# Kernel tuning notes

Measured on AMD Instinct MI355X. Metric: run time of the kernel, lower is better.

The kernel has to match this reference:

```python
import jax, jax.numpy as jnp
import numpy as np

D = 1024
POOL_SIZES = [1024, 512, 256, 128, 64]  # n_pos=32*32 -> n_codes=64
CODEBOOK_SIZE = 512
BATCH = 32
W_SCALE = 0.03125  # ~1/sqrt(D) so pre-softmax logits stay O(1)


def setup_inputs() -> dict:
    key = jax.random.key(0)
    ks = jax.random.split(key, 7)
    x = jax.random.normal(ks[0], (BATCH, POOL_SIZES[0], D), dtype=jnp.float32)
    queries = jax.random.normal(ks[1], (len(POOL_SIZES), POOL_SIZES[0], D), dtype=jnp.float32)
    wq = jax.random.normal(ks[2], (len(POOL_SIZES), D, D), dtype=jnp.float32) * W_SCALE
    wk = jax.random.normal(ks[3], (len(POOL_SIZES), D, D), dtype=jnp.float32) * W_SCALE
    wv = jax.random.normal(ks[4], (len(POOL_SIZES), D, D), dtype=jnp.float32) * W_SCALE
    wo = jax.random.normal(ks[5], (len(POOL_SIZES), D, D), dtype=jnp.float32) * W_SCALE
    codebook = jax.random.normal(ks[6], (CODEBOOK_SIZE, D), dtype=jnp.float32)
    return {"x": x, "queries": queries, "wq": wq, "wk": wk, "wv": wv, "wo": wo, "codebook": codebook}


def reference(x, queries, wq, wk, wv, wo, codebook):
    # StackedPooling: S -> 1024 -> 512 -> 256 -> 128 -> 64 via AttentionPool stages
    scale = D ** (-0.5)
    h = x
    for i, K in enumerate(POOL_SIZES):
        q = queries[i, :K, :] @ wq[i]              # [K, D] learned queries, q_proj
        k = jnp.einsum("bsd,de->bse", h, wk[i])    # [B, S, D]
        v = jnp.einsum("bsd,de->bse", h, wv[i])    # [B, S, D]
        logits = jnp.einsum("kd,bsd->bks", q, k) * scale
        attn = jax.nn.softmax(logits, axis=-1)     # [B, K, S]
        pooled = jnp.einsum("bks,bsd->bkd", attn, v)
        h = jnp.einsum("bkd,de->bke", pooled, wo[i])  # [B, K, D]
    # VQ codebook quantization: nearest code per latent (squared L2)
    z = h                                          # [B, n_codes, D]
    d2 = (jnp.sum(z * z, axis=-1, keepdims=True)
          - 2.0 * jnp.einsum("bkd,cd->bkc", z, codebook)
          + jnp.sum(codebook * codebook, axis=-1))  # [B, n_codes, C]
    idx = jnp.argmin(d2, axis=-1)                  # [B, n_codes] int
    z_q = codebook[idx]                            # [B, n_codes, D]
    # straight-through estimator
    out = z + jax.lax.stop_gradient(z_q - z)
    return out
```

## Files before the change

### kernel.cpp

```cpp
#include <hip/hip_runtime.h>


#define MB (1024ull * 1024ull)

typedef unsigned short u16;
typedef __attribute__((ext_vector_type(4))) float f32x4;
typedef __bf16 bf16x8 __attribute__((ext_vector_type(8)));

__device__ __forceinline__ u16 f2bf(float f) {
  unsigned u = __float_as_uint(f);
  unsigned r = u + 0x7FFFu + ((u >> 16) & 1u);
  return (u16)(r >> 16);
}
__device__ __forceinline__ float bf2f(u16 h) {
  return __uint_as_float(((unsigned)h) << 16);
}

typedef __attribute__((address_space(1))) const void GASV;
typedef __attribute__((address_space(3))) void LASV;
__device__ __forceinline__ void async16(const void* g, void* l) {
  __builtin_amdgcn_global_load_lds((GASV*)g, (LASV*)l, 16, 0, 0);
}

__device__ __forceinline__ int xcd_swz(int bid, int nwg) {
  const int q8 = nwg >> 3, r8 = nwg & 7;
  const int xcd = bid & 7, idx = bid >> 3;
  return (xcd < r8 ? xcd * (q8 + 1) : r8 * (q8 + 1) + (xcd - r8) * q8) + idx;
}

template<int MODE>
__global__ __launch_bounds__(512, 1)
void gemm_c(const u16* __restrict__ A, const u16* __restrict__ B,
            float* __restrict__ Cf, u16* __restrict__ Cb,
            int M, int N, int KLEN, int ld,
            long long sA, long long sB, long long sC, int ldc, float alpha,
            int nxt, int nyt)
{
  __shared__ u16 lds[65536];
  const int tid  = threadIdx.x;
  const int lane = tid & 63;
  const int w    = tid >> 6;
  const int wr   = w >> 2, wc = w & 3;

  const int wg = xcd_swz((int)blockIdx.x, (int)gridDim.x);
  const int bx = wg % nxt;
  const int by = (wg / nxt) % nyt;
  const int bz = wg / (nxt * nyt);

  const int m0 = by * 256, n0 = bx * 256;
  const u16* Ab = A + (size_t)bz * sA;
  const u16* Bb = B + (size_t)bz * sB;
  const int NT = KLEN >> 6;

  f32x4 acc[8][4] = {};

  const int Rl  = tid >> 2;
  const int sgs = (tid & 3) ^ ((tid >> 3) & 3);
  int ra0 = m0 + Rl;        ra0 = ra0 < M - 1 ? ra0 : M - 1;
  int ra1 = m0 + 128 + Rl;  ra1 = ra1 < M - 1 ? ra1 : M - 1;
  int rb0 = n0 + Rl;        rb0 = rb0 < N - 1 ? rb0 : N - 1;
  int rb1 = n0 + 128 + Rl;  rb1 = rb1 < N - 1 ? rb1 : N - 1;
  const u16* gA0 = Ab + (size_t)ra0 * ld + (sgs << 3);
  const u16* gA1 = Ab + (size_t)ra1 * ld + (sgs << 3);
  const u16* gB0 = Bb + (size_t)rb0 * ld + (sgs << 3);
  const u16* gB1 = Bb + (size_t)rb1 * ld + (sgs << 3);
  const int ldst = (w << 4) * 32;

  auto stageH = [&](int mat, int buf, int kh, int tile) {
    const int tt = tile < NT ? tile : NT - 1;
    const int kc = (tt << 6) + (kh << 5);
    u16* d = &lds[(mat << 15) + (buf << 14) + (kh << 13) + ldst];
    if (mat == 0) { async16(gA0 + kc, d); async16(gA1 + kc, d + 4096); }
    else          { async16(gB0 + kc, d); async16(gB1 + kc, d + 4096); }
  };

  const int rsel = lane & 15;
  const int ksub = lane >> 4;
  const int sw   = ksub ^ ((rsel >> 1) & 3);
  const u16* ldsA = &lds[(wr * 128 + rsel) * 32 + sw * 8];
  const u16* ldsB = &lds[32768 + (wc * 64 + rsel) * 32 + sw * 8];

  auto phase = [&](int buf, int kh, int mh, bf16x8* b,
                   int smat, int sbuf, int skh, int stile, int vm) {
    bf16x8 a[4];
    if (mh == 0) {
#pragma unroll
      for (int ni = 0; ni < 4; ++ni)
        b[ni] = *(const bf16x8*)&ldsB[buf * 16384 + kh * 8192 + ni * 512];
    }
#pragma unroll
    for (int mi = 0; mi < 4; ++mi)
      a[mi] = *(const bf16x8*)&ldsA[buf * 16384 + kh * 8192 + mh * 2048 + mi * 512];
    stageH(smat, sbuf, skh, stile);
    if (vm == 10)     asm volatile("s_waitcnt vmcnt(10)" ::: "memory");
    else if (vm == 6) asm volatile("s_waitcnt vmcnt(6)" ::: "memory");
    __builtin_amdgcn_s_barrier();
    asm volatile("s_waitcnt lgkmcnt(0)" ::: "memory");
    __builtin_amdgcn_sched_barrier(0);
    __builtin_amdgcn_s_setprio(1);
#pragma unroll
    for (int mi = 0; mi < 4; ++mi)
#pragma unroll
      for (int ni = 0; ni < 4; ++ni)
        acc[mh * 4 + mi][ni] = __builtin_amdgcn_mfma_f32_16x16x32_bf16(
            a[mi], b[ni], acc[mh * 4 + mi][ni], 0, 0, 0);
    __builtin_amdgcn_s_setprio(0);
    __builtin_amdgcn_s_barrier();
  };

  stageH(1, 0, 0, 0); stageH(0, 0, 0, 0); stageH(1, 0, 1, 0); stageH(0, 0, 1, 0);
  stageH(1, 1, 0, 1); stageH(0, 1, 0, 1); stageH(1, 1, 1, 1);
  asm volatile("s_waitcnt vmcnt(6)" ::: "memory");
  __builtin_amdgcn_s_barrier();

  const int NI = NT >> 1;
  for (int it = 0; it < NI; ++it) {
    const int t0 = it << 1, t1 = t0 + 1;
    bf16x8 b0[4], b1[4];
    phase(0, 0, 0, b0, 0, 1, 1, t1,     -1);
    phase(0, 0, 1, b0, 1, 0, 0, t0 + 2, -1);
    phase(0, 1, 0, b1, 0, 0, 0, t0 + 2, -1);
    phase(0, 1, 1, b1, 1, 0, 1, t0 + 2, 10);
    phase(1, 0, 0, b0, 0, 0, 1, t0 + 2, -1);
    phase(1, 0, 1, b0, 1, 1, 0, t1 + 2, 10);
    phase(1, 1, 0, b1, 0, 1, 0, t1 + 2, -1);
    phase(1, 1, 1, b1, 1, 1, 1, t1 + 2, 6);
  }
  asm volatile("s_waitcnt vmcnt(0)" ::: "memory");

#pragma unroll
  for (int mi = 0; mi < 8; ++mi)
#pragma unroll
    for (int ni = 0; ni < 4; ++ni)
#pragma unroll
      for (int i = 0; i < 4; ++i) {
        const int row = m0 + wr * 128 + mi * 16 + ((lane >> 4) << 2) + i;
        const int col = n0 + wc * 64 + ni * 16 + rsel;
        if (row < M && col < N) {
          const float v = acc[mi][ni][i] * alpha;
          const size_t off = (size_t)bz * sC + (size_t)row * ldc + col;
          if (MODE == 0) Cf[off] = v;
          else           Cb[off] = f2bf(v);
        }
      }
}

template<int MODE>
__global__ __launch_bounds__(256, 2)
void gemm_s(const u16* __restrict__ A, const u16* __restrict__ B,
            float* __restrict__ Cf, u16* __restrict__ Cb,
            int M, int N, int KLEN, int ld,
            long long sA, long long sB, long long sC, int ldc, float alpha,
            int nxt, int nyt)
{
  __shared__ u16 lds[32768];
  const int tid  = threadIdx.x;
  const int lane = tid & 63;
  const int w    = tid >> 6;
  const int wr   = w >> 1, wc = w & 1;

  const int wg = xcd_swz((int)blockIdx.x, (int)gridDim.x);
  const int bx = wg % nxt;
  const int by = (wg / nxt) % nyt;
  const int bz = wg / (nxt * nyt);

  const int m0 = by * 128, n0 = bx * 128;
  const u16* Ab = A + (size_t)bz * sA;
  const u16* Bb = B + (size_t)bz * sB;
  const int NT = KLEN >> 6;

  f32x4 acc[4][4] = {};

  const int Rl  = tid >> 3;
  const int sgs = (tid & 7) ^ (Rl & 7);
  const int ldst = (w << 3) * 64;

  auto stage = [&](int t, int buf) {
    const int kc = t << 6;
#pragma unroll
    for (int mat = 0; mat < 2; ++mat)
#pragma unroll
      for (int j = 0; j < 4; ++j) {
        int rg = (mat ? n0 : m0) + j * 32 + Rl;
        const int lim = (mat ? N : M) - 1;
        rg = rg < lim ? rg : lim;
        const u16* src = (mat ? Bb : Ab) + (size_t)rg * ld + kc + (sgs << 3);
        async16(src, &lds[(buf << 14) + (mat << 13) + j * 2048 + ldst]);
      }
  };

  const int rsel = lane & 15, ksub = lane >> 4;
  const int e  = rsel & 7;
  const int s0 = ((e >> 2) << 2) | (ksub ^ (e & 3));
  const int s1 = s0 ^ 4;
  const u16* ldsA0 = &lds[(wr * 64 + rsel) * 64 + s0 * 8];
  const u16* ldsA1 = &lds[(wr * 64 + rsel) * 64 + s1 * 8];
  const u16* ldsB0 = &lds[8192 + (wc * 64 + rsel) * 64 + s0 * 8];
  const u16* ldsB1 = &lds[8192 + (wc * 64 + rsel) * 64 + s1 * 8];

  stage(0, 0);
  for (int t = 0; t < NT; ++t) {
    const int buf = t & 1;
    if (t + 1 < NT) {
      stage(t + 1, buf ^ 1);
      asm volatile("s_waitcnt vmcnt(8)" ::: "memory");
    } else {
      asm volatile("s_waitcnt vmcnt(0)" ::: "memory");
    }
    __builtin_amdgcn_s_barrier();
    bf16x8 af[4][2], bf[4][2];
#pragma unroll
    for (int f = 0; f < 4; ++f) {
      af[f][0] = *(const bf16x8*)&ldsA0[buf * 16384 + f * 1024];
      af[f][1] = *(const bf16x8*)&ldsA1[buf * 16384 + f * 1024];
      bf[f][0] = *(const bf16x8*)&ldsB0[buf * 16384 + f * 1024];
      bf[f][1] = *(const bf16x8*)&ldsB1[buf * 16384 + f * 1024];
    }
    asm volatile("s_waitcnt lgkmcnt(0)" ::: "memory");
    __builtin_amdgcn_sched_barrier(0);
    __builtin_amdgcn_s_setprio(1);
#pragma unroll
    for (int mi = 0; mi < 4; ++mi)
#pragma unroll
      for (int ni = 0; ni < 4; ++ni)
#pragma unroll
        for (int kh = 0; kh < 2; ++kh)
          acc[mi][ni] = __builtin_amdgcn_mfma_f32_16x16x32_bf16(
              af[mi][kh], bf[ni][kh], acc[mi][ni], 0, 0, 0);
    __builtin_amdgcn_s_setprio(0);
    __builtin_amdgcn_s_barrier();
  }

#pragma unroll
  for (int mi = 0; mi < 4; ++mi)
#pragma unroll
    for (int ni = 0; ni < 4; ++ni)
#pragma unroll
      for (int i = 0; i < 4; ++i) {
        const int row = m0 + wr * 64 + mi * 16 + ((lane >> 4) << 2) + i;
        const int col = n0 + wc * 64 + ni * 16 + rsel;
        if (row < M && col < N) {
          const float v = acc[mi][ni][i] * alpha;
          const size_t off = (size_t)bz * sC + (size_t)row * ldc + col;
          if (MODE == 0) Cf[off] = v;
          else           Cb[off] = f2bf(v);
        }
      }
}

__global__ void multicast_k(const float* __restrict__ q, const float* __restrict__ wqp,
                            const float* __restrict__ wkp, const float* __restrict__ wvp,
                            const float* __restrict__ cbp,
                            u16* __restrict__ dq, u16* __restrict__ dwq,
                            u16* __restrict__ dwk, u16* __restrict__ dwv,
                            u16* __restrict__ dcb)
{
  long long i = (long long)blockIdx.x * 256 + threadIdx.x;
  const long long stride = (long long)gridDim.x * 256;
  for (; i < 5373952ll; i += stride) {
    const float* src; u16* dst; long long j;
    if (i < 1310720)      { src = q;   dst = dq;  j = i; }
    else if (i < 2621440) { src = wqp; dst = dwq; j = i - 1310720; }
    else if (i < 3932160) { src = wkp; dst = dwk; j = i - 2621440; }
    else if (i < 5242880) { src = wvp; dst = dwv; j = i - 3932160; }
    else                  { src = cbp; dst = dcb; j = i - 5242880; }
    const float4 v = *(const float4*)&src[j << 2];
    *(ushort4*)&dst[j << 2] = make_ushort4(f2bf(v.x), f2bf(v.y), f2bf(v.z), f2bf(v.w));
  }
}

__global__ __launch_bounds__(256)
void cast_trans_k(const float* __restrict__ in, u16* __restrict__ h,
                  u16* __restrict__ ht)
{
  __shared__ float t[32][33];
  const int z = blockIdx.z;
  const float* src = in + (size_t)z * 1048576;
  u16* dh = h  + (size_t)z * 1048576;
  u16* dt = ht + (size_t)z * 1048576;
  const int x0 = blockIdx.x * 32, y0 = blockIdx.y * 32;
  const int tx = threadIdx.x, ty = threadIdx.y;
#pragma unroll
  for (int k = 0; k < 4; ++k) {
    const float v = src[(size_t)(y0 + ty + 8 * k) * 1024 + (x0 + tx)];
    t[ty + 8 * k][tx] = v;
    dh[(size_t)(y0 + ty + 8 * k) * 1024 + (x0 + tx)] = f2bf(v);
  }
  __syncthreads();
#pragma unroll
  for (int k = 0; k < 4; ++k)
    dt[(size_t)(x0 + ty + 8 * k) * 1024 + (y0 + tx)] = f2bf(t[tx][ty + 8 * k]);
}

__global__ __launch_bounds__(256)
void transpose_cast_k(const float* __restrict__ in, u16* __restrict__ out)
{
  __shared__ float t[32][33];
  const int z = blockIdx.z;
  const float* src = in + (size_t)z * 1048576;
  u16* dst = out + (size_t)z * 1048576;
  const int x0 = blockIdx.x * 32, y0 = blockIdx.y * 32;
  const int tx = threadIdx.x, ty = threadIdx.y;
#pragma unroll
  for (int k = 0; k < 4; ++k)
    t[ty + 8 * k][tx] = src[(size_t)(y0 + ty + 8 * k) * 1024 + (x0 + tx)];
  __syncthreads();
#pragma unroll
  for (int k = 0; k < 4; ++k)
    dst[(size_t)(x0 + ty + 8 * k) * 1024 + (y0 + tx)] = f2bf(t[tx][ty + 8 * k]);
}

__global__ __launch_bounds__(256)
void transpose_u16_k(const u16* __restrict__ in, u16* __restrict__ out, int R)
{
  __shared__ u16 t[32][33];
  const size_t zi = (size_t)blockIdx.z * R * 1024;
  const size_t zo = (size_t)blockIdx.z * 1024 * R;
  const int x0 = blockIdx.x * 32, y0 = blockIdx.y * 32;
  const int tx = threadIdx.x, ty = threadIdx.y;
#pragma unroll
  for (int k = 0; k < 4; ++k)
    t[ty + 8 * k][tx] = in[zi + (size_t)(y0 + ty + 8 * k) * 1024 + (x0 + tx)];
  __syncthreads();
#pragma unroll
  for (int k = 0; k < 4; ++k)
    out[zo + (size_t)(x0 + ty + 8 * k) * R + (y0 + tx)] = t[tx][ty + 8 * k];
}

__global__ __launch_bounds__(256)
void softmax_b(const u16* __restrict__ lg, u16* __restrict__ at, int S)
{
  const size_t row = blockIdx.x;
  const u16* src = lg + row * S;
  const int tid = threadIdx.x;
  float v[4];
  float mx = -3.402823466e38f;
#pragma unroll
  for (int c = 0; c < 4; ++c) {
    const int j = tid + c * 256;
    v[c] = (j < S) ? bf2f(src[j]) : -3.402823466e38f;
    mx = fmaxf(mx, v[c]);
  }
#pragma unroll
  for (int o = 32; o > 0; o >>= 1) mx = fmaxf(mx, __shfl_xor(mx, o));
  __shared__ float rmx[4];
  if ((tid & 63) == 0) rmx[tid >> 6] = mx;
  __syncthreads();
  mx = fmaxf(fmaxf(rmx[0], rmx[1]), fmaxf(rmx[2], rmx[3]));
  float sum = 0.f;
#pragma unroll
  for (int c = 0; c < 4; ++c) { v[c] = expf(v[c] - mx); sum += v[c]; }
#pragma unroll
  for (int o = 32; o > 0; o >>= 1) sum += __shfl_xor(sum, o);
  __shared__ float rsm[4];
  if ((tid & 63) == 0) rsm[tid >> 6] = sum;
  __syncthreads();
  sum = rsm[0] + rsm[1] + rsm[2] + rsm[3];
  const float inv = 1.0f / sum;
  u16* dst = at + row * S;
#pragma unroll
  for (int c = 0; c < 4; ++c) {
    const int j = tid + c * 256;
    if (j < S) dst[j] = f2bf(v[c] * inv);
  }
}

__global__ __launch_bounds__(256)
void cnorm_kernel(const float* __restrict__ cb, float* __restrict__ cn)
{
  const int c = blockIdx.x;
  const float4 v = ((const float4*)(cb + (size_t)c * 1024))[threadIdx.x];
  float s = v.x * v.x + v.y * v.y + v.z * v.z + v.w * v.w;
#pragma unroll
  for (int o = 32; o > 0; o >>= 1) s += __shfl_xor(s, o);
  __shared__ float r4[4];
  if ((threadIdx.x & 63) == 0) r4[threadIdx.x >> 6] = s;
  __syncthreads();
  if (threadIdx.x == 0) cn[c] = r4[0] + r4[1] + r4[2] + r4[3];
}

__global__ __launch_bounds__(256)
void argmin_gather_k(const float* __restrict__ dot, const float* __restrict__ cn,
                     const float* __restrict__ cb, float* __restrict__ out)
{
  const size_t lat = blockIdx.x;
  const int tid = threadIdx.x;
  const float* dr = dot + lat * 512;
  float best = 3.402823466e38f;
  int bi = 0;
#pragma unroll
  for (int cc = 0; cc < 2; ++cc) {
    const int c = tid + cc * 256;
    const float sc = cn[c] - 2.0f * dr[c];
    if (sc < best || (sc == best && c < bi)) { best = sc; bi = c; }
  }
  __shared__ float rb[256];
  __shared__ int   ri[256];
  rb[tid] = best; ri[tid] = bi;
  __syncthreads();
  for (int s = 128; s > 0; s >>= 1) {
    if (tid < s) {
      const float ob = rb[tid + s];
      const int oi = ri[tid + s];
      if (ob < rb[tid] || (ob == rb[tid] && oi < ri[tid])) { rb[tid] = ob; ri[tid] = oi; }
    }
    __syncthreads();
  }
  const int sel = ri[0];
  ((float4*)(out + lat * 1024))[tid] = ((const float4*)(cb + (size_t)sel * 1024))[tid];
}

__global__ void fill_kernel(float* p, float v, int n) {
  const int i = blockIdx.x * 256 + threadIdx.x;
  if (i < n) p[i] = v;
}

static void gX(hipStream_t st, int mode,
               const u16* A, const u16* B, float* Cf, u16* Cb,
               int M, int N, int KLEN, int ld,
               long long sA, long long sB, long long sC, int ldc,
               int batch, float alpha)
{
  const int b256 = ((M + 255) / 256) * ((N + 255) / 256) * batch;
  if (b256 >= 192 && (KLEN & 127) == 0) {
    const int nxt = (N + 255) / 256, nyt = (M + 255) / 256;
    dim3 grid(nxt * nyt * batch), blk(512);
    if (mode == 0)
      gemm_c<0><<<grid, blk, 0, st>>>(A, B, Cf, Cb, M, N, KLEN, ld, sA, sB, sC, ldc, alpha, nxt, nyt);
    else
      gemm_c<1><<<grid, blk, 0, st>>>(A, B, Cf, Cb, M, N, KLEN, ld, sA, sB, sC, ldc, alpha, nxt, nyt);
  } else {
    const int nxt = (N + 127) / 128, nyt = (M + 127) / 128;
    dim3 grid(nxt * nyt * batch), blk(256);
    if (mode == 0)
      gemm_s<0><<<grid, blk, 0, st>>>(A, B, Cf, Cb, M, N, KLEN, ld, sA, sB, sC, ldc, alpha, nxt, nyt);
    else
      gemm_s<1><<<grid, blk, 0, st>>>(A, B, Cf, Cb, M, N, KLEN, ld, sA, sB, sC, ldc, alpha, nxt, nyt);
  }
}

extern "C" void kernel_launch(void* const* d_in, const int* in_sizes, int n_in,
                              void* d_out, int out_size, void* d_ws, size_t ws_size,
                              hipStream_t stream)
{
  const float* x   = (const float*)d_in[0];
  const float* qry = (const float*)d_in[1];
  const float* wq  = (const float*)d_in[2];
  const float* wk  = (const float*)d_in[3];
  const float* wv  = (const float*)d_in[4];
  const float* wo  = (const float*)d_in[5];
  const float* cb  = (const float*)d_in[6];
  float* out = (float*)d_out;

  const size_t NEED = 312 * MB;
  if (ws_size < NEED) {
    fill_kernel<<<(out_size + 255) / 256, 256, 0, stream>>>(out, (float)ws_size, out_size);
    return;
  }
  char* ws = (char*)d_ws;
  const long long W = 1048576;
  u16*  QKb   = (u16*)(ws + 0 * MB);
  u16*  WqkTb = (u16*)(ws + 10 * MB);
  u16*  WVOb  = (u16*)(ws + 20 * MB);
  u16*  CBb   = (u16*)(ws + 30 * MB);
  float* CN   = (float*)(ws + 31 * MB);
  u16*  QKP   = (u16*)(ws + 32 * MB);
  u16*  WCb   = (u16*)(ws + 40 * MB);
  u16*  WC5   = (u16*)(ws + 48 * MB);
  u16*  CBW   = (u16*)(ws + 50 * MB);
  float* DOT  = (float*)(ws + 51 * MB);
  u16*  U    = (u16*)(ws + 56 * MB);
  u16*  UT   = (u16*)(ws + 120 * MB);
  u16*  ATb  = (u16*)(ws + 184 * MB);
  u16*  LOG  = (u16*)(ws + 248 * MB);
  u16*  QSb  = (u16*)(ws + 56 * MB);
  u16*  WQb  = (u16*)(ws + 66 * MB);
  u16*  WVb  = (u16*)(ws + 76 * MB);
  u16*  WKb  = (u16*)(ws + 86 * MB);
  u16*  WOTb = (u16*)(ws + 96 * MB);

  const int S_in[5]  = {1024, 1024, 512, 256, 128};
  const int K_out[5] = {1024, 512, 256, 128, 64};

  multicast_k<<<2048, 256, 0, stream>>>(qry, wq, wk, wv, cb,
                                        QSb, WQb, WKb, WVb, CBb);
  dim3 tb(32, 8), tg5(32, 32, 5);
  transpose_cast_k<<<tg5, tb, 0, stream>>>(wo, WOTb);
  cnorm_kernel<<<512, 256, 0, stream>>>(cb, CN);

  gX(stream, 1, WKb, WQb, nullptr, WqkTb,
     1024, 1024, 1024, 1024, W, W, W, 1024, 10, 1.0f);
  gX(stream, 1, QSb, WqkTb, nullptr, QKb,
     1024, 1024, 1024, 1024, W, W, W, 1024, 5, 1.0f);

  {
    dim3 tgt(32, 32, 1);
    transpose_u16_k<<<tgt, tb, 0, stream>>>(WVOb, WCb, 1024);
  }
  gX(stream, 1, WCb,         WVOb + 1 * W, nullptr, WCb + 1 * W, 1024, 1024, 1024, 1024, 0, 0, 0, 1024, 1, 1.0f);
  gX(stream, 1, WCb + 1 * W, WVOb + 2 * W, nullptr, WCb + 2 * W, 1024, 1024, 1024, 1024, 0, 0, 0, 1024, 1, 1.0f);
  gX(stream, 1, WCb + 2 * W, WVOb + 3 * W, nullptr, WCb + 3 * W, 1024, 1024, 1024, 1024, 0, 0, 0, 1024, 1, 1.0f);
  gX(stream, 1, WCb + 3 * W, WVOb + 4 * W, nullptr, WC5,         1024, 1024, 1024, 1024, 0, 0, 0, 1024, 1, 1.0f);
  gX(stream, 1, QKb + W, WCb, nullptr, QKP,
     1024, 1024, 1024, 1024, W, W, W, 1024, 4, 1.0f);
  gX(stream, 1, CBb, WC5, nullptr, CBW,
     512, 1024, 1024, 1024, 0, 0, 0, 1024, 1, 1.0f);

  dim3 tgx(32, 32, 32);
  cast_trans_k<<<tgx, tb, 0, stream>>>(x, U, UT);

  for (int i = 0; i < 5; ++i) {
    const int S = S_in[i], KO = K_out[i];
    const u16* qk = (i == 0) ? QKb : QKP + (size_t)(i - 1) * W;

    gX(stream, 1, qk, U, nullptr, LOG,
       KO, S, 1024, 1024, 0, (long long)S * 1024, (long long)KO * S, S, 32, 0.03125f);
    softmax_b<<<32 * KO, 256, 0, stream>>>(LOG, ATb, S);
    gX(stream, 1, ATb, UT, nullptr, U,
       KO, 1024, S, S, (long long)KO * S, (long long)1024 * S,
       (long long)KO * 1024, 1024, 32, 1.0f);
    if (i < 4) {
      dim3 tgt(32, KO / 32, 32);
      transpose_u16_k<<<tgt, tb, 0, stream>>>(U, UT, KO);
    }
  }

  gX(stream, 0, U, CBW, DOT, nullptr,
     2048, 512, 1024, 1024, 0, 0, 0, 512, 1, 1.0f);
  argmin_gather_k<<<2048, 256, 0, stream>>>(DOT, CN, cb, out);
}
```

Measured before the change: 703.0 us.

## Add 64x64-tile GEMM for small grids and drop a per-phase barrier

Adds a gemm_t kernel that uses 64x64 output tiles and double-buffered async LDS loads. It is dispatched whenever the 128-tile grid would have fewer than 192 workgroups, so the small late-stage GEMMs fill more CUs. It also removes the pre-MFMA barrier and lgkmcnt wait in the big gemm_c phase loop, keeping only a sched_barrier after the trailing barrier. Without that wait, the MFMAs could read LDS data before the loads have completed, unless the compiler inserts the wait itself.

```diff
diff --git a/kernel.cpp b/kernel.cpp
--- a/kernel.cpp
+++ b/kernel.cpp
@@ -94,9 +94,6 @@
     stageH(smat, sbuf, skh, stile);
     if (vm == 10)     asm volatile("s_waitcnt vmcnt(10)" ::: "memory");
     else if (vm == 6) asm volatile("s_waitcnt vmcnt(6)" ::: "memory");
-    __builtin_amdgcn_s_barrier();
-    asm volatile("s_waitcnt lgkmcnt(0)" ::: "memory");
-    __builtin_amdgcn_sched_barrier(0);
     __builtin_amdgcn_s_setprio(1);
 #pragma unroll
     for (int mi = 0; mi < 4; ++mi)
@@ -106,12 +103,14 @@
             a[mi], b[ni], acc[mh * 4 + mi][ni], 0, 0, 0);
     __builtin_amdgcn_s_setprio(0);
     __builtin_amdgcn_s_barrier();
+    __builtin_amdgcn_sched_barrier(0);
   };
 
   stageH(1, 0, 0, 0); stageH(0, 0, 0, 0); stageH(1, 0, 1, 0); stageH(0, 0, 1, 0);
   stageH(1, 1, 0, 1); stageH(0, 1, 0, 1); stageH(1, 1, 1, 1);
   asm volatile("s_waitcnt vmcnt(6)" ::: "memory");
   __builtin_amdgcn_s_barrier();
+  __builtin_amdgcn_sched_barrier(0);
 
   const int NI = NT >> 1;
   for (int it = 0; it < NI; ++it) {
@@ -248,6 +247,105 @@
       }
 }
 
+template<int MODE>
+__global__ __launch_bounds__(256, 4)
+void gemm_t(const u16* __restrict__ A, const u16* __restrict__ B,
+            float* __restrict__ Cf, u16* __restrict__ Cb,
+            int M, int N, int KLEN, int ld,
+            long long sA, long long sB, long long sC, int ldc, float alpha,
+            int nxt, int nyt)
+{
+  __shared__ u16 lds[16384];
+  const int tid  = threadIdx.x;
+  const int lane = tid & 63;
+  const int w    = tid >> 6;
+  const int wr   = w >> 1, wc = w & 1;
+
+  const int wg = xcd_swz((int)blockIdx.x, (int)gridDim.x);
+  const int bx = wg % nxt;
+  const int by = (wg / nxt) % nyt;
+  const int bz = wg / (nxt * nyt);
+
+  const int m0 = by * 64, n0 = bx * 64;
+  const u16* Ab = A + (size_t)bz * sA;
+  const u16* Bb = B + (size_t)bz * sB;
+  const int NT = KLEN >> 6;
+
+  f32x4 acc[2][2] = {};
+
+  const int Rl  = tid >> 3;
+  const int sgs = (tid & 7) ^ (Rl & 7);
+
+  auto stage = [&](int t, int buf) {
+    const int kc = t << 6;
+#pragma unroll
+    for (int j = 0; j < 4; ++j) {
+      const int mat = j >> 1, rh = j & 1;
+      int rg = (mat ? n0 : m0) + rh * 32 + Rl;
+      const int lim = (mat ? N : M) - 1;
+      rg = rg < lim ? rg : lim;
+      const u16* src = (mat ? Bb : Ab) + (size_t)rg * ld + kc + (sgs << 3);
+      async16(src, &lds[(buf << 13) + (mat << 12) + (rh * 32 + w * 8) * 64]);
+    }
+  };
+
+  const int rsel = lane & 15, ksub = lane >> 4;
+  const int e  = rsel & 7;
+  const int s0 = ((e >> 2) << 2) | (ksub ^ (e & 3));
+  const int s1 = s0 ^ 4;
+  const u16* lA0 = &lds[(wr * 32 + rsel) * 64 + s0 * 8];
+  const u16* lA1 = &lds[(wr * 32 + rsel) * 64 + s1 * 8];
+  const u16* lB0 = &lds[4096 + (wc * 32 + rsel) * 64 + s0 * 8];
+  const u16* lB1 = &lds[4096 + (wc * 32 + rsel) * 64 + s1 * 8];
+
+  stage(0, 0);
+  for (int t = 0; t < NT; ++t) {
+    const int buf = t & 1;
+    if (t + 1 < NT) {
+      stage(t + 1, buf ^ 1);
+      asm volatile("s_waitcnt vmcnt(4)" ::: "memory");
+    } else {
+      asm volatile("s_waitcnt vmcnt(0)" ::: "memory");
+    }
+    __builtin_amdgcn_s_barrier();
+    bf16x8 af[2][2], bg[2][2];
+#pragma unroll
+    for (int f = 0; f < 2; ++f) {
+      af[f][0] = *(const bf16x8*)&lA0[buf * 8192 + f * 1024];
+      af[f][1] = *(const bf16x8*)&lA1[buf * 8192 + f * 1024];
+      bg[f][0] = *(const bf16x8*)&lB0[buf * 8192 + f * 1024];
+      bg[f][1] = *(const bf16x8*)&lB1[buf * 8192 + f * 1024];
+    }
+    __builtin_amdgcn_s_setprio(1);
+#pragma unroll
+    for (int mi = 0; mi < 2; ++mi)
+#pragma unroll
+      for (int ni = 0; ni < 2; ++ni)
+#pragma unroll
+        for (int kh = 0; kh < 2; ++kh)
+          acc[mi][ni] = __builtin_amdgcn_mfma_f32_16x16x32_bf16(
+              af[mi][kh], bg[ni][kh], acc[mi][ni], 0, 0, 0);
+    __builtin_amdgcn_s_setprio(0);
+    __builtin_amdgcn_s_barrier();
+  }
+
+#pragma unroll
+  for (int mi = 0; mi < 2; ++mi)
+#pragma unroll
+    for (int ni = 0; ni < 2; ++ni)
+#pragma unroll
+      for (int i = 0; i < 4; ++i) {
+        const int row = m0 + wr * 32 + mi * 16 + ((lane >> 4) << 2) + i;
+        const int col = n0 + wc * 32 + ni * 16 + rsel;
+        if (row < M && col < N) {
+          const float v = acc[mi][ni][i] * alpha;
+          const size_t off = (size_t)bz * sC + (size_t)row * ldc + col;
+          if (MODE == 0) Cf[off] = v;
+          else           Cb[off] = f2bf(v);
+        }
+      }
+}
+
 __global__ void multicast_k(const float* __restrict__ q, const float* __restrict__ wqp,
                             const float* __restrict__ wkp, const float* __restrict__ wvp,
                             const float* __restrict__ cbp,
@@ -422,6 +520,7 @@
                int batch, float alpha)
 {
   const int b256 = ((M + 255) / 256) * ((N + 255) / 256) * batch;
+  const int b128 = ((M + 127) / 128) * ((N + 127) / 128) * batch;
   if (b256 >= 192 && (KLEN & 127) == 0) {
     const int nxt = (N + 255) / 256, nyt = (M + 255) / 256;
     dim3 grid(nxt * nyt * batch), blk(512);
@@ -429,6 +528,13 @@
       gemm_c<0><<<grid, blk, 0, st>>>(A, B, Cf, Cb, M, N, KLEN, ld, sA, sB, sC, ldc, alpha, nxt, nyt);
     else
       gemm_c<1><<<grid, blk, 0, st>>>(A, B, Cf, Cb, M, N, KLEN, ld, sA, sB, sC, ldc, alpha, nxt, nyt);
+  } else if (b128 < 192) {
+    const int nxt = (N + 63) / 64, nyt = (M + 63) / 64;
+    dim3 grid(nxt * nyt * batch), blk(256);
+    if (mode == 0)
+      gemm_t<0><<<grid, blk, 0, st>>>(A, B, Cf, Cb, M, N, KLEN, ld, sA, sB, sC, ldc, alpha, nxt, nyt);
+    else
+      gemm_t<1><<<grid, blk, 0, st>>>(A, B, Cf, Cb, M, N, KLEN, ld, sA, sB, sC, ldc, alpha, nxt, nyt);
   } else {
     const int nxt = (N + 127) / 128, nyt = (M + 127) / 128;
     dim3 grid(nxt * nyt * batch), blk(256);
```

New measurement: 660.3 us (median of 2 runs). -6.1%, faster.

## Replace 256x256 and 128x128 GEMM kernels with smaller-tile 128 and 64 variants

Applied to the files above, without the earlier changes.

The large 256x256 eight-wave GEMM with its interleaved half-tile pipeline is replaced by a 128x128 four-wave kernel with 32-wide K steps and a simple double buffer. The fallback 128x128 kernel becomes 64x64 with smaller LDS and higher occupancy. Dispatch thresholds change to match. The aim is more blocks and higher occupancy for the small, batched GEMMs in the pooling stack, in exchange for less data reuse per tile and a simpler, less tuned pipeline on the large GEMMs.

```diff
diff --git a/kernel.cpp b/kernel.cpp
--- a/kernel.cpp
+++ b/kernel.cpp
@@ -29,112 +29,90 @@
 }
 
 template<int MODE>
-__global__ __launch_bounds__(512, 1)
-void gemm_c(const u16* __restrict__ A, const u16* __restrict__ B,
+__global__ __launch_bounds__(256, 3)
+void gemm_m(const u16* __restrict__ A, const u16* __restrict__ B,
             float* __restrict__ Cf, u16* __restrict__ Cb,
             int M, int N, int KLEN, int ld,
             long long sA, long long sB, long long sC, int ldc, float alpha,
             int nxt, int nyt)
 {
-  __shared__ u16 lds[65536];
+  __shared__ u16 lds[16384];
   const int tid  = threadIdx.x;
   const int lane = tid & 63;
   const int w    = tid >> 6;
-  const int wr   = w >> 2, wc = w & 3;
+  const int wr   = w >> 1, wc = w & 1;
 
   const int wg = xcd_swz((int)blockIdx.x, (int)gridDim.x);
   const int bx = wg % nxt;
   const int by = (wg / nxt) % nyt;
   const int bz = wg / (nxt * nyt);
 
-  const int m0 = by * 256, n0 = bx * 256;
+  const int m0 = by * 128, n0 = bx * 128;
   const u16* Ab = A + (size_t)bz * sA;
   const u16* Bb = B + (size_t)bz * sB;
-  const int NT = KLEN >> 6;
-
-  f32x4 acc[8][4] = {};
-
-  const int Rl  = tid >> 2;
+  const int NT = KLEN >> 5;
+
+  f32x4 acc[4][4] = {};
+
+  const int Rq  = tid >> 2;
   const int sgs = (tid & 3) ^ ((tid >> 3) & 3);
-  int ra0 = m0 + Rl;        ra0 = ra0 < M - 1 ? ra0 : M - 1;
-  int ra1 = m0 + 128 + Rl;  ra1 = ra1 < M - 1 ? ra1 : M - 1;
-  int rb0 = n0 + Rl;        rb0 = rb0 < N - 1 ? rb0 : N - 1;
-  int rb1 = n0 + 128 + Rl;  rb1 = rb1 < N - 1 ? rb1 : N - 1;
+  int ra0 = m0 + Rq;       ra0 = ra0 < M - 1 ? ra0 : M - 1;
+  int ra1 = m0 + 64 + Rq;  ra1 = ra1 < M - 1 ? ra1 : M - 1;
+  int rb0 = n0 + Rq;       rb0 = rb0 < N - 1 ? rb0 : N - 1;
+  int rb1 = n0 + 64 + Rq;  rb1 = rb1 < N - 1 ? rb1 : N - 1;
   const u16* gA0 = Ab + (size_t)ra0 * ld + (sgs << 3);
   const u16* gA1 = Ab + (size_t)ra1 * ld + (sgs << 3);
   const u16* gB0 = Bb + (size_t)rb0 * ld + (sgs << 3);
   const u16* gB1 = Bb + (size_t)rb1 * ld + (sgs << 3);
   const int ldst = (w << 4) * 32;
 
-  auto stageH = [&](int mat, int buf, int kh, int tile) {
-    const int tt = tile < NT ? tile : NT - 1;
-    const int kc = (tt << 6) + (kh << 5);
-    u16* d = &lds[(mat << 15) + (buf << 14) + (kh << 13) + ldst];
-    if (mat == 0) { async16(gA0 + kc, d); async16(gA1 + kc, d + 4096); }
-    else          { async16(gB0 + kc, d); async16(gB1 + kc, d + 4096); }
+  auto stage = [&](int t, int buf) {
+    const int kc = t << 5;
+    u16* d = &lds[(buf << 13) + ldst];
+    async16(gA0 + kc, d);
+    async16(gA1 + kc, d + 2048);
+    async16(gB0 + kc, d + 4096);
+    async16(gB1 + kc, d + 6144);
   };
 
   const int rsel = lane & 15;
   const int ksub = lane >> 4;
   const int sw   = ksub ^ ((rsel >> 1) & 3);
-  const u16* ldsA = &lds[(wr * 128 + rsel) * 32 + sw * 8];
-  const u16* ldsB = &lds[32768 + (wc * 64 + rsel) * 32 + sw * 8];
-
-  auto phase = [&](int buf, int kh, int mh, bf16x8* b,
-                   int smat, int sbuf, int skh, int stile, int vm) {
-    bf16x8 a[4];
-    if (mh == 0) {
+  const u16* ldsA = &lds[(wr * 64 + rsel) * 32 + sw * 8];
+  const u16* ldsB = &lds[4096 + (wc * 64 + rsel) * 32 + sw * 8];
+
+  stage(0, 0);
+  if (NT > 1) stage(1, 1);
+  for (int t = 0; t < NT; ++t) {
+    const int buf = t & 1;
+    if (t + 1 < NT) asm volatile("s_waitcnt vmcnt(4)" ::: "memory");
+    else            asm volatile("s_waitcnt vmcnt(0)" ::: "memory");
+    __builtin_amdgcn_s_barrier();
+    bf16x8 a[4], b[4];
+#pragma unroll
+    for (int f = 0; f < 4; ++f) {
+      a[f] = *(const bf16x8*)&ldsA[buf * 8192 + f * 512];
+      b[f] = *(const bf16x8*)&ldsB[buf * 8192 + f * 512];
+    }
+    __builtin_amdgcn_s_setprio(1);
+#pragma unroll
+    for (int mi = 0; mi < 4; ++mi)
 #pragma unroll
       for (int ni = 0; ni < 4; ++ni)
-        b[ni] = *(const bf16x8*)&ldsB[buf * 16384 + kh * 8192 + ni * 512];
-    }
-#pragma unroll
-    for (int mi = 0; mi < 4; ++mi)
-      a[mi] = *(const bf16x8*)&ldsA[buf * 16384 + kh * 8192 + mh * 2048 + mi * 512];
-    stageH(smat, sbuf, skh, stile);
-    if (vm == 10)     asm volatile("s_waitcnt vmcnt(10)" ::: "memory");
-    else if (vm == 6) asm volatile("s_waitcnt vmcnt(6)" ::: "memory");
-    __builtin_amdgcn_s_barrier();
-    asm volatile("s_waitcnt lgkmcnt(0)" ::: "memory");
-    __builtin_amdgcn_sched_barrier(0);
-    __builtin_amdgcn_s_setprio(1);
-#pragma unroll
-    for (int mi = 0; mi < 4; ++mi)
-#pragma unroll
-      for (int ni = 0; ni < 4; ++ni)
-        acc[mh * 4 + mi][ni] = __builtin_amdgcn_mfma_f32_16x16x32_bf16(
-            a[mi], b[ni], acc[mh * 4 + mi][ni], 0, 0, 0);
+        acc[mi][ni] = __builtin_amdgcn_mfma_f32_16x16x32_bf16(
+            a[mi], b[ni], acc[mi][ni], 0, 0, 0);
     __builtin_amdgcn_s_setprio(0);
     __builtin_amdgcn_s_barrier();
-  };
-
-  stageH(1, 0, 0, 0); stageH(0, 0, 0, 0); stageH(1, 0, 1, 0); stageH(0, 0, 1, 0);
-  stageH(1, 1, 0, 1); stageH(0, 1, 0, 1); stageH(1, 1, 1, 1);
-  asm volatile("s_waitcnt vmcnt(6)" ::: "memory");
-  __builtin_amdgcn_s_barrier();
-
-  const int NI = NT >> 1;
-  for (int it = 0; it < NI; ++it) {
-    const int t0 = it << 1, t1 = t0 + 1;
-    bf16x8 b0[4], b1[4];
-    phase(0, 0, 0, b0, 0, 1, 1, t1,     -1);
-    phase(0, 0, 1, b0, 1, 0, 0, t0 + 2, -1);
-    phase(0, 1, 0, b1, 0, 0, 0, t0 + 2, -1);
-    phase(0, 1, 1, b1, 1, 0, 1, t0 + 2, 10);
-    phase(1, 0, 0, b0, 0, 0, 1, t0 + 2, -1);
-    phase(1, 0, 1, b0, 1, 1, 0, t1 + 2, 10);
-    phase(1, 1, 0, b1, 0, 1, 0, t1 + 2, -1);
-    phase(1, 1, 1, b1, 1, 1, 1, t1 + 2, 6);
-  }
-  asm volatile("s_waitcnt vmcnt(0)" ::: "memory");
-
-#pragma unroll
-  for (int mi = 0; mi < 8; ++mi)
+    if (t + 2 < NT) stage(t + 2, buf);
+  }
+
+#pragma unroll
+  for (int mi = 0; mi < 4; ++mi)
 #pragma unroll
     for (int ni = 0; ni < 4; ++ni)
 #pragma unroll
       for (int i = 0; i < 4; ++i) {
-        const int row = m0 + wr * 128 + mi * 16 + ((lane >> 4) << 2) + i;
+        const int row = m0 + wr * 64 + mi * 16 + ((lane >> 4) << 2) + i;
         const int col = n0 + wc * 64 + ni * 16 + rsel;
         if (row < M && col < N) {
           const float v = acc[mi][ni][i] * alpha;
@@ -146,14 +124,14 @@
 }
 
 template<int MODE>
-__global__ __launch_bounds__(256, 2)
-void gemm_s(const u16* __restrict__ A, const u16* __restrict__ B,
+__global__ __launch_bounds__(256, 4)
+void gemm_t(const u16* __restrict__ A, const u16* __restrict__ B,
             float* __restrict__ Cf, u16* __restrict__ Cb,
             int M, int N, int KLEN, int ld,
             long long sA, long long sB, long long sC, int ldc, float alpha,
             int nxt, int nyt)
 {
-  __shared__ u16 lds[32768];
+  __shared__ u16 lds[16384];
   const int tid  = threadIdx.x;
   const int lane = tid & 63;
   const int w    = tid >> 6;
@@ -164,81 +142,77 @@
   const int by = (wg / nxt) % nyt;
   const int bz = wg / (nxt * nyt);
 
-  const int m0 = by * 128, n0 = bx * 128;
+  const int m0 = by * 64, n0 = bx * 64;
   const u16* Ab = A + (size_t)bz * sA;
   const u16* Bb = B + (size_t)bz * sB;
   const int NT = KLEN >> 6;
 
-  f32x4 acc[4][4] = {};
+  f32x4 acc[2][2] = {};
 
   const int Rl  = tid >> 3;
   const int sgs = (tid & 7) ^ (Rl & 7);
-  const int ldst = (w << 3) * 64;
 
   auto stage = [&](int t, int buf) {
     const int kc = t << 6;
 #pragma unroll
-    for (int mat = 0; mat < 2; ++mat)
-#pragma unroll
-      for (int j = 0; j < 4; ++j) {
-        int rg = (mat ? n0 : m0) + j * 32 + Rl;
-        const int lim = (mat ? N : M) - 1;
-        rg = rg < lim ? rg : lim;
-        const u16* src = (mat ? Bb : Ab) + (size_t)rg * ld + kc + (sgs << 3);
-        async16(src, &lds[(buf << 14) + (mat << 13) + j * 2048 + ldst]);
-      }
+    for (int j = 0; j < 4; ++j) {
+      const int mat = j >> 1, rh = j & 1;
+      int rg = (mat ? n0 : m0) + rh * 32 + Rl;
+      const int lim = (mat ? N : M) - 1;
+      rg = rg < lim ? rg : lim;
+      const u16* src = (mat ? Bb : Ab) + (size_t)rg * ld + kc + (sgs << 3);
+      async16(src, &lds[(buf << 13) + (mat << 12) + (rh * 32 + w * 8) * 64]);
+    }
   };
 
   const int rsel = lane & 15, ksub = lane >> 4;
   const int e  = rsel & 7;
   const int s0 = ((e >> 2) << 2) | (ksub ^ (e & 3));
   const int s1 = s0 ^ 4;
-  const u16* ldsA0 = &lds[(wr * 64 + rsel) * 64 + s0 * 8];
-  const u16* ldsA1 = &lds[(wr * 64 + rsel) * 64 + s1 * 8];
-  const u16* ldsB0 = &lds[8192 + (wc * 64 + rsel) * 64 + s0 * 8];
-  const u16* ldsB1 = &lds[8192 + (wc * 64 + rsel) * 64 + s1 * 8];
+  const u16* lA0 = &lds[(wr * 32 + rsel) * 64 + s0 * 8];
+  const u16* lA1 = &lds[(wr * 32 + rsel) * 64 + s1 * 8];
+  const u16* lB0 = &lds[4096 + (wc * 32 + rsel) * 64 + s0 * 8];
+  const u16* lB1 = &lds[4096 + (wc * 32 + rsel) * 64 + s1 * 8];
 
   stage(0, 0);
   for (int t = 0; t < NT; ++t) {
     const int buf = t & 1;
     if (t + 1 < NT) {
       stage(t + 1, buf ^ 1);
-      asm volatile("s_waitcnt vmcnt(8)" ::: "memory");
+      asm volatile("s_waitcnt vmcnt(4)" ::: "memory");
     } else {
       asm volatile("s_waitcnt vmcnt(0)" ::: "memory");
     }
     __builtin_amdgcn_s_barrier();
-    bf16x8 af[4][2], bf[4][2];
-#pragma unroll
-    for (int f = 0; f < 4; ++f) {
-      af[f][0] = *(const bf16x8*)&ldsA0[buf * 16384 + f * 1024];
-      af[f][1] = *(const bf16x8*)&ldsA1[buf * 16384 + f * 1024];
-      bf[f][0] = *(const bf16x8*)&ldsB0[buf * 16384 + f * 1024];
-      bf[f][1] = *(const bf16x8*)&ldsB1[buf * 16384 + f * 1024];
+    bf16x8 af[2][2], bg[2][2];
+#pragma unroll
+    for (int f = 0; f < 2; ++f) {
+      af[f][0] = *(const bf16x8*)&lA0[buf * 8192 + f * 1024];
+      af[f][1] = *(const bf16x8*)&lA1[buf * 8192 + f * 1024];
+      bg[f][0] = *(const bf16x8*)&lB0[buf * 8192 + f * 1024];
+      bg[f][1] = *(const bf16x8*)&lB1[buf * 8192 + f * 1024];
     }
-    asm volatile("s_waitcnt lgkmcnt(0)" ::: "memory");
-    __builtin_amdgcn_sched_barrier(0);
     __builtin_amdgcn_s_setprio(1);
 #pragma unroll
-    for (int mi = 0; mi < 4; ++mi)
-#pragma unroll
-      for (int ni = 0; ni < 4; ++ni)
+    for (int mi = 0; mi < 2; ++mi)
+#pragma unroll
+      for (int ni = 0; ni < 2; ++ni)
 #pragma unroll
         for (int kh = 0; kh < 2; ++kh)
           acc[mi][ni] = __builtin_amdgcn_mfma_f32_16x16x32_bf16(
-              af[mi][kh], bf[ni][kh], acc[mi][ni], 0, 0, 0);
+              af[mi][kh], bg[ni][kh], acc[mi][ni], 0, 0, 0);
     __builtin_amdgcn_s_setprio(0);
     __builtin_amdgcn_s_barrier();
   }
 
 #pragma unroll
-  for (int mi = 0; mi < 4; ++mi)
-#pragma unroll
-    for (int ni = 0; ni < 4; ++ni)
+  for (int mi = 0; mi < 2; ++mi)
+#pragma unroll
+    for (int ni = 0; ni < 2; ++ni)
 #pragma unroll
       for (int i = 0; i < 4; ++i) {
-        const int row = m0 + wr * 64 + mi * 16 + ((lane >> 4) << 2) + i;
-        const int col = n0 + wc * 64 + ni * 16 + rsel;
+        const int row = m0 + wr * 32 + mi * 16 + ((lane >> 4) << 2) + i;
+        const int col = n0 + wc * 32 + ni * 16 + rsel;
         if (row < M && col < N) {
           const float v = acc[mi][ni][i] * alpha;
           const size_t off = (size_t)bz * sC + (size_t)row * ldc + col;
@@ -421,21 +395,21 @@
                long long sA, long long sB, long long sC, int ldc,
                int batch, float alpha)
 {
-  const int b256 = ((M + 255) / 256) * ((N + 255) / 256) * batch;
-  if (b256 >= 192 && (KLEN & 127) == 0) {
-    const int nxt = (N + 255) / 256, nyt = (M + 255) / 256;
-    dim3 grid(nxt * nyt * batch), blk(512);
-    if (mode == 0)
-      gemm_c<0><<<grid, blk, 0, st>>>(A, B, Cf, Cb, M, N, KLEN, ld, sA, sB, sC, ldc, alpha, nxt, nyt);
-    else
-      gemm_c<1><<<grid, blk, 0, st>>>(A, B, Cf, Cb, M, N, KLEN, ld, sA, sB, sC, ldc, alpha, nxt, nyt);
-  } else {
+  const int b128 = ((M + 127) / 128) * ((N + 127) / 128) * batch;
+  if (b128 >= 192 && M >= 128 && (KLEN & 63) == 0) {
     const int nxt = (N + 127) / 128, nyt = (M + 127) / 128;
     dim3 grid(nxt * nyt * batch), blk(256);
     if (mode == 0)
-      gemm_s<0><<<grid, blk, 0, st>>>(A, B, Cf, Cb, M, N, KLEN, ld, sA, sB, sC, ldc, alpha, nxt, nyt);
+      gemm_m<0><<<grid, blk, 0, st>>>(A, B, Cf, Cb, M, N, KLEN, ld, sA, sB, sC, ldc, alpha, nxt, nyt);
     else
-      gemm_s<1><<<grid, blk, 0, st>>>(A, B, Cf, Cb, M, N, KLEN, ld, sA, sB, sC, ldc, alpha, nxt, nyt);
+      gemm_m<1><<<grid, blk, 0, st>>>(A, B, Cf, Cb, M, N, KLEN, ld, sA, sB, sC, ldc, alpha, nxt, nyt);
+  } else {
+    const int nxt = (N + 63) / 64, nyt = (M + 63) / 64;
+    dim3 grid(nxt * nyt * batch), blk(256);
+    if (mode == 0)
+      gemm_t<0><<<grid, blk, 0, st>>>(A, B, Cf, Cb, M, N, KLEN, ld, sA, sB, sC, ldc, alpha, nxt, nyt);
+    else
+      gemm_t<1><<<grid, blk, 0, st>>>(A, B, Cf, Cb, M, N, KLEN, ld, sA, sB, sC, ldc, alpha, nxt, nyt);
   }
 }
 
```

Result: no change. 703.8 us (+0.1%).
